# Performance work log

Measured on AMD Instinct MI355X. Metric: run time of the kernel, lower is better.

## Reference

```python
import jax, jax.numpy as jnp
import numpy as np

H = 16          # num_heads
BASE = 10000.0  # lrpe base
EPS = 1e-6      # rmsnorm eps


def setup_inputs() -> dict:
    key = jax.random.key(0)
    ks = jax.random.split(key, 8)
    b, n, d = 2, 2048, 1024
    hd = d // H
    s = 1.0 / np.sqrt(d)
    x = jax.random.normal(ks[0], (b, n, d), jnp.float32)
    wq = jax.random.normal(ks[1], (d, d), jnp.float32) * s
    wk = jax.random.normal(ks[2], (d, d), jnp.float32) * s
    wv = jax.random.normal(ks[3], (d, d), jnp.float32) * s
    wo = jax.random.normal(ks[4], (d, d), jnp.float32) * s
    wg1 = jax.random.normal(ks[5], (d, hd), jnp.float32) * s
    wg2 = jax.random.normal(ks[6], (hd, d), jnp.float32) * (1.0 / np.sqrt(hd))
    norm_w = jnp.ones((d,), jnp.float32)
    return {"x": x, "wq": wq, "wk": wk, "wv": wv, "wo": wo,
            "wg1": wg1, "wg2": wg2, "norm_w": norm_w}


def reference(x, wq, wk, wv, wo, wg1, wg2, norm_w):
    b, n, d = x.shape
    hd = d // H
    # projections + activations
    q = jax.nn.silu(x @ wq).reshape(b, n, H, hd)
    k = (x @ wk).reshape(b, n, H, hd)
    v = (x @ wv).reshape(b, n, H, hd)
    # vector decay via logcumsumexp over time (lse_state starts at 0 -> z[:,0]=0)
    f = jnp.concatenate([jnp.zeros((b, 1, H, hd), x.dtype), k], axis=1)  # (b,n+1,h,d)
    z = jax.lax.cumlogsumexp(f, axis=1)
    log_f = z[:, :-1] - z[:, 1:]          # (b,n,h,d), <= 0
    k = jnp.exp(k - z[:, 1:])             # normalized exp kernel keys
    # LRPE type 1 (cosine): d -> 2d, per-head theta slice
    theta = BASE ** (-2.0 / (H * hd) * jnp.arange(H * hd, dtype=x.dtype))
    theta = theta.reshape(H, hd)
    ang = jnp.arange(n, dtype=x.dtype)[:, None, None] * theta[None]  # (n,h,d)
    c, s_ = jnp.cos(ang), jnp.sin(ang)
    q = jnp.concatenate([q * c, q * s_], axis=-1)   # (b,n,h,2d)
    k = jnp.concatenate([k * c, k * s_], axis=-1)
    ld = jnp.concatenate([log_f, log_f], axis=-1)   # repeat '... d -> ... (g d)', g=2
    # lightning linear attention with vector decay: S_t = diag(exp(ld_t)) S_{t-1} + k_t v_t^T
    def step(S, inp):
        qt, kt, vt, lt = inp
        S = jnp.exp(lt)[..., None] * S + kt[..., None] * vt[..., None, :]
        o = jnp.einsum('bhe,bhev->bhv', qt, S)
        return S, o
    S0 = jnp.zeros((b, H, 2 * hd, hd), x.dtype)
    seq = (jnp.moveaxis(q, 1, 0), jnp.moveaxis(k, 1, 0),
           jnp.moveaxis(v, 1, 0), jnp.moveaxis(ld, 1, 0))
    _, o = jax.lax.scan(step, S0, seq)
    o = jnp.moveaxis(o, 0, 1).reshape(b, n, d)
    # fused gated group-RMSNorm (gate_pos='pre', sigmoid gate, num_groups=H)
    gate = (x @ wg1) @ wg2
    g = o * jax.nn.sigmoid(gate)
    gg = g.reshape(b, n, H, hd)
    rms = jnp.sqrt(jnp.mean(gg * gg, axis=-1, keepdims=True) + EPS)
    normed = (gg / rms).reshape(b, n, d) * norm_w
    return normed @ wo
```

## Files before the change

kernel.cpp:

```cpp
#include <hip/hip_runtime.h>
#include <math.h>

#define NH 16
#define HD 64
#define DMODEL 1024
#define NSEQ 2048
#define BATCH 2
#define CHUNK 32
#define NCH (NSEQ / CHUNK)
#define LN_BASE 9.210340371976184f

typedef __attribute__((ext_vector_type(8))) short bf16x8;
typedef __attribute__((ext_vector_type(8))) unsigned short u16x8;
typedef __attribute__((ext_vector_type(4))) float f32x4;

__device__ __forceinline__ unsigned short f2bf(float f) {
  union { float f; unsigned int u; } v; v.f = f;
  unsigned int u = v.u;
  unsigned int r = u + 0x7FFFu + ((u >> 16) & 1u);
  return (unsigned short)(r >> 16);
}
__device__ __forceinline__ float bf2f(unsigned short u) {
  union { unsigned int u; float f; } v; v.u = ((unsigned int)u) << 16;
  return v.f;
}

__device__ __forceinline__ void fast_sincos(float ang, float* s, float* c) {
  const float INV2PI = 0.15915494309189535f;
  const float TWOPI  = 6.283185307179586f;
  float rev = ang * INV2PI;
  rev = rev - floorf(rev);
  float ar = rev * TWOPI;
  *s = __sinf(ar);
  *c = __cosf(ar);
}

__device__ __forceinline__ void gload_lds16(const unsigned short* g,
                                            unsigned short* l) {
  __builtin_amdgcn_global_load_lds(
      (const __attribute__((address_space(1))) void*)g,
      (__attribute__((address_space(3))) void*)l, 16, 0, 0);
}

__global__ __launch_bounds__(256) void transpose_cvt6(
    const float* __restrict__ s0, const float* __restrict__ s1,
    const float* __restrict__ s2, const float* __restrict__ s3,
    const float* __restrict__ s4, const float* __restrict__ xs,
    unsigned short* __restrict__ d0, unsigned short* __restrict__ d1,
    unsigned short* __restrict__ d2, unsigned short* __restrict__ d3,
    unsigned short* __restrict__ d4, unsigned short* __restrict__ xd) {
  const int z = blockIdx.z;
  if (z == 5) {
    const int lin = blockIdx.y * 32 + blockIdx.x;
    const size_t base = (size_t)lin * 4096 + threadIdx.x * 4;
#pragma unroll
    for (int r = 0; r < 4; ++r) {
      float4 v = *(const float4*)(xs + base + r * 1024);
      unsigned short* o = xd + base + r * 1024;
      o[0] = f2bf(v.x); o[1] = f2bf(v.y); o[2] = f2bf(v.z); o[3] = f2bf(v.w);
    }
    return;
  }
  const float* in = (z == 0) ? s0 : (z == 1) ? s1 : (z == 2) ? s2
                    : (z == 3) ? s3 : s4;
  unsigned short* out = (z == 0) ? d0 : (z == 1) ? d1 : (z == 2) ? d2
                        : (z == 3) ? d3 : d4;
  __shared__ float tl[32][33];
  const int t = threadIdx.x;
  const int ci = t & 31, ri = t >> 5;
  const int br = blockIdx.y * 32, bc = blockIdx.x * 32;
#pragma unroll
  for (int rr = 0; rr < 4; ++rr)
    tl[ri + rr * 8][ci] = in[(size_t)(br + ri + rr * 8) * DMODEL + bc + ci];
  __syncthreads();
#pragma unroll
  for (int rr = 0; rr < 4; ++rr) {
    const int orow = bc + ri + rr * 8;
    const int ocol = br + ci;
    out[(size_t)orow * DMODEL + ocol] = f2bf(tl[ci][ri + rr * 8]);
  }
}

__global__ __launch_bounds__(256) void wg_gemm(const float* __restrict__ A,
                                               const float* __restrict__ B,
                                               float* __restrict__ C) {
  __shared__ float As[64][65];
  __shared__ float Bs[64][64];
  const int tid = threadIdx.x;
  const int tx = tid & 15, ty = tid >> 4;
  const int bm = (blockIdx.x >> 4) * 64;
  const int bn = (blockIdx.x & 15) * 64;

  {
    const int row = tid >> 2;
    const int ko = (tid & 3) * 16;
    const float* src = A + (size_t)(bm + row) * 64 + ko;
#pragma unroll
    for (int q = 0; q < 4; ++q) {
      float4 v = *(const float4*)(src + q * 4);
      As[row][ko + q * 4 + 0] = v.x; As[row][ko + q * 4 + 1] = v.y;
      As[row][ko + q * 4 + 2] = v.z; As[row][ko + q * 4 + 3] = v.w;
    }
  }
  {
    const int k = tid >> 2;
    const int co = (tid & 3) * 16;
    const float* src = B + (size_t)k * DMODEL + bn + co;
#pragma unroll
    for (int q = 0; q < 4; ++q)
      *(float4*)&Bs[k][co + q * 4] = *(const float4*)(src + q * 4);
  }
  __syncthreads();

  float acc[4][4];
#pragma unroll
  for (int i = 0; i < 4; ++i)
#pragma unroll
    for (int j = 0; j < 4; ++j) acc[i][j] = 0.f;
#pragma unroll 8
  for (int kk = 0; kk < 64; ++kk) {
    float a[4], b[4];
#pragma unroll
    for (int i = 0; i < 4; ++i) a[i] = As[ty * 4 + i][kk];
#pragma unroll
    for (int j = 0; j < 4; ++j) b[j] = Bs[kk][tx * 4 + j];
#pragma unroll
    for (int i = 0; i < 4; ++i)
#pragma unroll
      for (int j = 0; j < 4; ++j) acc[i][j] = fmaf(a[i], b[j], acc[i][j]);
  }
#pragma unroll
  for (int i = 0; i < 4; ++i) {
    float4 r = make_float4(acc[i][0], acc[i][1], acc[i][2], acc[i][3]);
    *(float4*)&C[(size_t)(bm + ty * 4 + i) * DMODEL + bn + tx * 4] = r;
  }
}

__global__ __launch_bounds__(256, 6) void gemm_bf16_fused(
    const unsigned short* __restrict__ A, const unsigned short* __restrict__ Bt,
    unsigned short* __restrict__ B0, unsigned short* __restrict__ B1,
    unsigned short* __restrict__ B2, unsigned short* __restrict__ B3,
    int M, int Ntot, int K) {
  __shared__ unsigned short As[64][64];
  __shared__ unsigned short Bs[128][64];
  const int tid = threadIdx.x;
  const int l = tid & 63;
  const int w = tid >> 6;
  const int wr = (w >> 1) * 32;
  const int wc = (w & 1) * 64;

  const int orig = blockIdx.x;
  const int xcd = orig & 7;
  const int idx = orig >> 3;
  const int bm = ((xcd >> 1) * 16 + (idx & 15)) * 64;
  const int bn = ((xcd & 1) * 16 + (idx >> 4)) * 128;

  const int lrow = l >> 3;
  const int cd = l & 7;
  const int cl = cd ^ lrow;

  f32x4 acc[2][4];
#pragma unroll
  for (int m = 0; m < 2; ++m)
#pragma unroll
    for (int n = 0; n < 4; ++n) acc[m][n] = (f32x4){0.f, 0.f, 0.f, 0.f};

  for (int k0 = 0; k0 < K; k0 += 64) {
    __syncthreads();
#pragma unroll
    for (int c = 0; c < 2; ++c) {
      const int row = w * 16 + c * 8 + lrow;
      unsigned short* la = (unsigned short*)As + (w * 16 + c * 8) * 64 + l * 8;
      gload_lds16(A + (size_t)(bm + row) * K + k0 + cl * 8, la);
    }
#pragma unroll
    for (int c = 0; c < 4; ++c) {
      const int row = w * 32 + c * 8 + lrow;
      unsigned short* lb = (unsigned short*)Bs + (w * 32 + c * 8) * 64 + l * 8;
      gload_lds16(Bt + (size_t)(bn + row) * K + k0 + cl * 8, lb);
    }
    __syncthreads();

#pragma unroll
    for (int ks = 0; ks < 2; ++ks) {
      bf16x8 af[2], bfr[4];
#pragma unroll
      for (int m = 0; m < 2; ++m) {
        const int r = wr + m * 16 + (l & 15);
        const int phys = (ks * 4 + (l >> 4)) ^ (r & 7);
        af[m] = *(const bf16x8*)&As[r][phys * 8];
      }
#pragma unroll
      for (int n = 0; n < 4; ++n) {
        const int r = wc + n * 16 + (l & 15);
        const int phys = (ks * 4 + (l >> 4)) ^ (r & 7);
        bfr[n] = *(const bf16x8*)&Bs[r][phys * 8];
      }
#pragma unroll
      for (int m = 0; m < 2; ++m)
#pragma unroll
        for (int n = 0; n < 4; ++n)
          acc[m][n] = __builtin_amdgcn_mfma_f32_16x16x32_bf16(af[m], bfr[n], acc[m][n], 0, 0, 0);
    }
  }

#pragma unroll
  for (int m = 0; m < 2; ++m) {
    const int row0 = bm + wr + m * 16 + (l >> 4) * 4;
#pragma unroll
    for (int n = 0; n < 4; ++n) {
      const int colw = wc + n * 16 + (l & 15);
#pragma unroll
      for (int r = 0; r < 4; ++r) {
        float x = acc[m][n][r];
        const int nb = bn >> 10;
        unsigned short* Bb = (nb == 0) ? B0 : (nb == 1) ? B1 : (nb == 2) ? B2 : B3;
        const int col = (bn & 1023) + colw;
        if (nb == 0) x = x / (1.f + expf(-x));
        Bb[(size_t)(row0 + r) * DMODEL + col] = f2bf(x);
      }
    }
  }
}

__global__ __launch_bounds__(256, 6) void gemm_bf16_wo(
    const unsigned short* __restrict__ A, const unsigned short* __restrict__ Bt,
    float* __restrict__ C, int M, int N, int K) {
  __shared__ unsigned short As[32][64];
  __shared__ unsigned short Bs[128][64];
  const int tid = threadIdx.x;
  const int l = tid & 63;
  const int w = tid >> 6;
  const int wr = (w >> 1) * 16;
  const int wc = (w & 1) * 64;

  const int nwg = gridDim.x;
  const int orig = blockIdx.x;
  const int swz = (orig & 7) * (nwg >> 3) + (orig >> 3);
  const int ntn = N >> 7;
  const int bm = (swz / ntn) * 32;
  const int bn = (swz % ntn) * 128;

  const int lrow = l >> 3;
  const int cd = l & 7;
  const int cl = cd ^ lrow;

  f32x4 acc[4];
#pragma unroll
  for (int n = 0; n < 4; ++n) acc[n] = (f32x4){0.f, 0.f, 0.f, 0.f};

  for (int k0 = 0; k0 < K; k0 += 64) {
    __syncthreads();
    {
      const int row = w * 8 + lrow;
      unsigned short* la = (unsigned short*)As + (w * 8) * 64 + l * 8;
      gload_lds16(A + (size_t)(bm + row) * K + k0 + cl * 8, la);
    }
#pragma unroll
    for (int c = 0; c < 4; ++c) {
      const int row = w * 32 + c * 8 + lrow;
      unsigned short* lb = (unsigned short*)Bs + (w * 32 + c * 8) * 64 + l * 8;
      gload_lds16(Bt + (size_t)(bn + row) * K + k0 + cl * 8, lb);
    }
    __syncthreads();

#pragma unroll
    for (int ks = 0; ks < 2; ++ks) {
      bf16x8 af, bfr[4];
      {
        const int r = wr + (l & 15);
        const int phys = (ks * 4 + (l >> 4)) ^ (r & 7);
        af = *(const bf16x8*)&As[r][phys * 8];
      }
#pragma unroll
      for (int n = 0; n < 4; ++n) {
        const int r = wc + n * 16 + (l & 15);
        const int phys = (ks * 4 + (l >> 4)) ^ (r & 7);
        bfr[n] = *(const bf16x8*)&Bs[r][phys * 8];
      }
#pragma unroll
      for (int n = 0; n < 4; ++n)
        acc[n] = __builtin_amdgcn_mfma_f32_16x16x32_bf16(af, bfr[n], acc[n], 0, 0, 0);
    }
  }

  {
    const int row0 = bm + wr + (l >> 4) * 4;
#pragma unroll
    for (int n = 0; n < 4; ++n) {
      const int col = bn + wc + n * 16 + (l & 15);
#pragma unroll
      for (int r = 0; r < 4; ++r)
        C[(size_t)(row0 + r) * N + col] = acc[n][r];
    }
  }
}

template <int ACT>
__global__ __launch_bounds__(256) void gemm_f32(const float* __restrict__ A,
                                                const float* __restrict__ B,
                                                float* __restrict__ C,
                                                int M, int N, int K) {
  __shared__ __align__(16) float As[16][128];
  __shared__ __align__(16) float Bs[16][128];
  const int tid = threadIdx.x;
  const int tx = tid & 15;
  const int ty = tid >> 4;
  const int bm = blockIdx.y * 128;
  const int bn = blockIdx.x * 128;

  float acc[8][8];
#pragma unroll
  for (int i = 0; i < 8; ++i)
#pragma unroll
    for (int j = 0; j < 8; ++j) acc[i][j] = 0.f;

  for (int k0 = 0; k0 < K; k0 += 16) {
    {
      const int row = tid >> 1;
      const int ko = (tid & 1) * 8;
      const float* src = A + (size_t)(bm + row) * K + k0 + ko;
      float4 a0 = *(const float4*)src;
      float4 a1 = *(const float4*)(src + 4);
      As[ko + 0][row] = a0.x; As[ko + 1][row] = a0.y;
      As[ko + 2][row] = a0.z; As[ko + 3][row] = a0.w;
      As[ko + 4][row] = a1.x; As[ko + 5][row] = a1.y;
      As[ko + 6][row] = a1.z; As[ko + 7][row] = a1.w;
    }
    {
      const int kr = tid >> 4;
      const int no = (tid & 15) * 8;
      float4 b0 = make_float4(0.f, 0.f, 0.f, 0.f);
      float4 b1 = b0;
      if (no < N) {
        const float* src = B + (size_t)(k0 + kr) * N + bn + no;
        b0 = *(const float4*)src;
        b1 = *(const float4*)(src + 4);
      }
      *(float4*)&Bs[kr][no] = b0;
      *(float4*)&Bs[kr][no + 4] = b1;
    }
    __syncthreads();
#pragma unroll
    for (int kk = 0; kk < 16; ++kk) {
      float a[8], b[8];
      *(float4*)&a[0] = *(const float4*)&As[kk][ty * 8];
      *(float4*)&a[4] = *(const float4*)&As[kk][ty * 8 + 4];
      *(float4*)&b[0] = *(const float4*)&Bs[kk][tx * 8];
      *(float4*)&b[4] = *(const float4*)&Bs[kk][tx * 8 + 4];
#pragma unroll
      for (int i = 0; i < 8; ++i)
#pragma unroll
        for (int j = 0; j < 8; ++j) acc[i][j] = fmaf(a[i], b[j], acc[i][j]);
    }
    __syncthreads();
  }

#pragma unroll
  for (int i = 0; i < 8; ++i) {
    const int row = bm + ty * 8 + i;
#pragma unroll
    for (int j = 0; j < 8; j += 4) {
      const int col = bn + tx * 8 + j;
      if (col < N) {
        float4 r;
        float* rv = (float*)&r;
#pragma unroll
        for (int q = 0; q < 4; ++q) {
          float x = acc[i][j + q];
          if (ACT == 1) x = x / (1.f + expf(-x));
          rv[q] = x;
        }
        *(float4*)&C[(size_t)row * N + col] = r;
      }
    }
  }
}

__global__ __launch_bounds__(256) void chunk_partial(
    const unsigned short* __restrict__ kb, float* __restrict__ partial) {
  const int blk = blockIdx.x;
  const int b = blk >> 8;
  const int rem = blk & 255;
  const int c = rem >> 2;
  const int seg = rem & 3;
  const int ch = seg * 256 + threadIdx.x;
  const unsigned short* base = kb + ((size_t)(b * NSEQ + c * CHUNK)) * DMODEL + ch;
  float acc = 0.f;
  for (int s = 0; s < CHUNK; ++s)
    acc += expf(bf2f(base[(size_t)s * DMODEL]));
  partial[((size_t)(b * NCH + c)) * DMODEL + ch] = acc;
}

__global__ __launch_bounds__(256) void chunk_zoff(const float* __restrict__ partial,
                                                  float* __restrict__ zoff) {
  const int g = blockIdx.x * 256 + threadIdx.x;
  const int b = g >> 10, dd = g & 1023;
  const size_t base = (size_t)b * NCH * DMODEL + dd;
  float vals[NCH];
#pragma unroll
  for (int c = 0; c < NCH; ++c)
    vals[c] = partial[base + (size_t)c * DMODEL];
  float run = 1.0f;
#pragma unroll
  for (int c = 0; c < NCH; ++c) {
    zoff[base + (size_t)c * DMODEL] = run;
    run += vals[c];
  }
}

__global__ __launch_bounds__(256) void chunk_attn(
    const unsigned short* __restrict__ qb, const unsigned short* __restrict__ kb,
    const unsigned short* __restrict__ vb, const float* __restrict__ zoff,
    unsigned short* __restrict__ qp, unsigned short* __restrict__ G,
    unsigned short* __restrict__ ob) {
  const int bidx = blockIdx.x;
  const int bh = bidx / NCH, c = bidx % NCH;
  const int b = bh >> 4, h = bh & 15;
  const int c0 = h * HD;

  __shared__ float sk[CHUNK][64];
  __shared__ float ps[4][64];
  __shared__ __align__(16) unsigned short qplds[CHUNK][136];
  __shared__ __align__(16) unsigned short khlds[CHUNK][136];
  __shared__ __align__(16) unsigned short kht[128][40];
  __shared__ __align__(16) unsigned short vt[64][40];
  __shared__ __align__(16) unsigned short slds[CHUNK][40];

  const int tid = threadIdx.x;
  const int l = tid & 63;
  const int w = tid >> 6;

  for (int idx = tid; idx < CHUNK * 64; idx += 256) {
    const int s = idx >> 6, dd2 = idx & 63;
    const size_t g = ((size_t)(b * NSEQ + c * CHUNK + s)) * DMODEL + c0 + dd2;
    sk[s][dd2] = bf2f(kb[g]);
    vt[dd2][s] = vb[g];
  }
  __syncthreads();

  const int dd = l;
  const int wq_ = w;
  {
    float a = 0.f;
#pragma unroll
    for (int i = 0; i < CHUNK / 4; ++i) a += expf(sk[wq_ * (CHUNK / 4) + i][dd]);
    ps[wq_][dd] = a;
  }
  __syncthreads();
  {
    float z = zoff[((size_t)(b * NCH + c)) * DMODEL + c0 + dd];
    for (int q2 = 0; q2 < wq_; ++q2) z += ps[q2][dd];
    const float theta = expf(-2.0f * (float)(c0 + dd) * (1.0f / 1024.0f) * LN_BASE);
#pragma unroll 2
    for (int i = 0; i < CHUNK / 4; ++i) {
      const int s = wq_ * (CHUNK / 4) + i;
      const int t = c * CHUNK + s;
      const float ek = expf(sk[s][dd]);
      z += ek;
      float sn, cs_;
      fast_sincos((float)t * theta, &sn, &cs_);
      const float qv = bf2f(qb[((size_t)(b * NSEQ + t)) * DMODEL + c0 + dd]);
      const float inv = 1.0f / z;
      const unsigned short kcb = f2bf(ek * cs_);
      const unsigned short ksb = f2bf(ek * sn);
      const unsigned short qcb = f2bf(qv * cs_ * inv);
      const unsigned short qsb = f2bf(qv * sn * inv);
      khlds[s][dd] = kcb;
      khlds[s][64 + dd] = ksb;
      kht[dd][s] = kcb;
      kht[64 + dd][s] = ksb;
      qplds[s][dd] = qcb;
      qplds[s][64 + dd] = qsb;
      unsigned short* qpo = qp + ((size_t)bidx * CHUNK + s) * 128;
      qpo[dd] = qcb;
      qpo[64 + dd] = qsb;
    }
  }
  __syncthreads();

  {
    const int mw = w >> 1, nw = w & 1;
    f32x4 sd = (f32x4){0.f, 0.f, 0.f, 0.f};
#pragma unroll
    for (int ks = 0; ks < 4; ++ks) {
      bf16x8 aq = *(const bf16x8*)&qplds[mw * 16 + (l & 15)][(l >> 4) * 8 + ks * 32];
      bf16x8 bk = *(const bf16x8*)&khlds[nw * 16 + (l & 15)][(l >> 4) * 8 + ks * 32];
      sd = __builtin_amdgcn_mfma_f32_16x16x32_bf16(aq, bk, sd, 0, 0, 0);
    }
    const int trow = mw * 16 + (l >> 4) * 4;
    const int scol = nw * 16 + (l & 15);
#pragma unroll
    for (int r = 0; r < 4; ++r) {
      const float v = (scol <= trow + r) ? sd[r] : 0.f;
      slds[trow + r][scol] = f2bf(v);
    }
  }

  {
    unsigned short* go = G + (size_t)bidx * 8192;
    const bf16x8 bv = *(const bf16x8*)&vt[w * 16 + (l & 15)][(l >> 4) * 8];
    const int jc = w * 16 + (l & 15);
#pragma unroll
    for (int et = 0; et < 8; ++et) {
      bf16x8 ak = *(const bf16x8*)&kht[et * 16 + (l & 15)][(l >> 4) * 8];
      f32x4 gd = (f32x4){0.f, 0.f, 0.f, 0.f};
      gd = __builtin_amdgcn_mfma_f32_16x16x32_bf16(ak, bv, gd, 0, 0, 0);
      const int e0r = et * 16 + (l >> 4) * 4;
#pragma unroll
      for (int r = 0; r < 4; ++r) go[(e0r + r) * 64 + jc] = f2bf(gd[r]);
    }
  }
  __syncthreads();

  {
    const bf16x8 bv = *(const bf16x8*)&vt[w * 16 + (l & 15)][(l >> 4) * 8];
    const int jc = w * 16 + (l & 15);
#pragma unroll
    for (int tt = 0; tt < 2; ++tt) {
      bf16x8 as = *(const bf16x8*)&slds[tt * 16 + (l & 15)][(l >> 4) * 8];
      f32x4 od = (f32x4){0.f, 0.f, 0.f, 0.f};
      od = __builtin_amdgcn_mfma_f32_16x16x32_bf16(as, bv, od, 0, 0, 0);
      const int trow = tt * 16 + (l >> 4) * 4;
#pragma unroll
      for (int r = 0; r < 4; ++r)
        ob[((size_t)(b * NSEQ + c * CHUNK + trow + r)) * DMODEL + c0 + jc] = f2bf(od[r]);
    }
  }
}

__global__ __launch_bounds__(256) void chunk_prefix(unsigned short* __restrict__ G) {
  const int g = blockIdx.x * 256 + threadIdx.x;
  const int bh = g >> 12;
  const int e2 = (g & 4095) * 2;
  unsigned int* base = (unsigned int*)(G + (size_t)bh * NCH * 8192 + e2);
  unsigned int vals[NCH];
#pragma unroll
  for (int c = 0; c < NCH; ++c)
    vals[c] = base[(size_t)c * 4096];
  float run0 = 0.f, run1 = 0.f;
#pragma unroll
  for (int c = 0; c < NCH; ++c) {
    base[(size_t)c * 4096] =
        (unsigned int)f2bf(run0) | ((unsigned int)f2bf(run1) << 16);
    run0 += bf2f((unsigned short)(vals[c] & 0xFFFFu));
    run1 += bf2f((unsigned short)(vals[c] >> 16));
  }
}

__global__ __launch_bounds__(256) void chunk_inter_norm(
    const unsigned short* __restrict__ qp, const unsigned short* __restrict__ S0,
    const unsigned short* __restrict__ ob, const unsigned short* __restrict__ gate,
    const float* __restrict__ norm_w, unsigned short* __restrict__ outb) {
  const int bidx = blockIdx.x;
  const int bh = bidx / NCH, c = bidx % NCH;
  const int b = bh >> 4, h = bh & 15;
  const int c0 = h * HD;

  __shared__ float s0l[128][68];
  __shared__ float qpl[CHUNK][132];

  const int tid = threadIdx.x;
  {
    const unsigned short* src = S0 + (size_t)bidx * 8192;
    for (int idx = tid * 8; idx < 8192; idx += 2048) {
      const int e = idx >> 6, j = idx & 63;
      u16x8 v8 = *(const u16x8*)(src + idx);
#pragma unroll
      for (int q = 0; q < 8; ++q) s0l[e][j + q] = bf2f(v8[q]);
    }
    const unsigned short* qsrc = qp + (size_t)bidx * CHUNK * 128;
    for (int idx = tid * 8; idx < CHUNK * 128; idx += 2048) {
      const int t = idx >> 7, e = idx & 127;
      u16x8 v8 = *(const u16x8*)(qsrc + idx);
#pragma unroll
      for (int q = 0; q < 8; ++q) qpl[t][e + q] = bf2f(v8[q]);
    }
  }
  __syncthreads();

  const int t = tid >> 3;
  const int j0 = (tid & 7) * 8;
  float acc[8] = {0, 0, 0, 0, 0, 0, 0, 0};
#pragma unroll 4
  for (int e = 0; e < 128; ++e) {
    const float a = qpl[t][e];
#pragma unroll
    for (int j = 0; j < 8; ++j) acc[j] = fmaf(a, s0l[e][j0 + j], acc[j]);
  }

  const size_t rowoff = ((size_t)(b * NSEQ + c * CHUNK + t)) * DMODEL + c0 + j0;
  u16x8 oi = *(const u16x8*)(ob + rowoff);
  u16x8 gt = *(const u16x8*)(gate + rowoff);
  float g[8];
  float ss = 0.f;
#pragma unroll
  for (int q = 0; q < 8; ++q) {
    const float o = acc[q] + bf2f(oi[q]);
    const float gv = bf2f(gt[q]);
    g[q] = o / (1.f + expf(-gv));
    ss = fmaf(g[q], g[q], ss);
  }
  ss += __shfl_xor(ss, 1);
  ss += __shfl_xor(ss, 2);
  ss += __shfl_xor(ss, 4);
  const float rms = sqrtf(ss * (1.0f / 64.0f) + 1e-6f);
  const float inv = 1.0f / rms;
  u16x8 outv;
#pragma unroll
  for (int q = 0; q < 8; ++q)
    outv[q] = f2bf(g[q] * inv * norm_w[c0 + j0 + q]);
  *(u16x8*)(outb + rowoff) = outv;
}

__global__ __launch_bounds__(256) void scan_kernel(const float* __restrict__ qb,
                                                   const float* __restrict__ kb,
                                                   const float* __restrict__ vb,
                                                   float* __restrict__ ob) {
  const int bh = blockIdx.x;
  const int b = bh >> 4;
  const int h = bh & 15;
  const int c0 = h * HD;

  __shared__ float sk[64][64];
  __shared__ float sq[64][64];
  __shared__ float sv[64][64];
  __shared__ float kh[128];
  __shared__ float qph[128];
  __shared__ float vsh[64];
  __shared__ float opart[4][64];

  const int tid = threadIdx.x;
  const int lane = tid & 63;
  const int w = tid >> 6;
  const int e0 = w * 32;

  float T[32];
#pragma unroll
  for (int i = 0; i < 32; ++i) T[i] = 0.f;

  float zrun = 1.0f;
  float theta_v = 0.f;
  if (tid < 64) theta_v = expf(-2.0f * (float)(c0 + tid) * (1.0f / 1024.0f) * LN_BASE);

  for (int t0 = 0; t0 < NSEQ; t0 += 64) {
    __syncthreads();
    for (int idx = tid; idx < 64 * 64; idx += 256) {
      const int tl = idx >> 6;
      const int dd = idx & 63;
      const size_t g = ((size_t)(b * NSEQ + t0 + tl)) * DMODEL + c0 + dd;
      sk[tl][dd] = kb[g];
      sq[tl][dd] = qb[g];
      sv[tl][dd] = vb[g];
    }
    __syncthreads();

    for (int tl = 0; tl < 64; ++tl) {
      const int t = t0 + tl;
      if (tid < 64) {
        const int dd = tid;
        const float kr = sk[tl][dd];
        const float ek = expf(kr);
        zrun += ek;
        const float inv = 1.0f / zrun;
        float cs_, sn;
        fast_sincos((float)t * theta_v, &sn, &cs_);
        const float qv = sq[tl][dd];
        kh[dd] = ek * cs_;
        kh[64 + dd] = ek * sn;
        qph[dd] = qv * cs_ * inv;
        qph[64 + dd] = qv * sn * inv;
        vsh[dd] = sv[tl][dd];
      }
      __syncthreads();

      const float vj = vsh[lane];
      float accj = 0.f;
#pragma unroll
      for (int i = 0; i < 32; ++i) {
        T[i] = fmaf(kh[e0 + i], vj, T[i]);
        accj = fmaf(qph[e0 + i], T[i], accj);
      }
      opart[w][lane] = accj;
      __syncthreads();

      if (tid < 64) {
        const float o = opart[0][tid] + opart[1][tid] + opart[2][tid] + opart[3][tid];
        ob[((size_t)(b * NSEQ + t)) * DMODEL + c0 + tid] = o;
      }
    }
  }
}

__global__ __launch_bounds__(256) void gated_rmsnorm_f32(
    const float* __restrict__ o, const float* __restrict__ gate,
    const float* __restrict__ norm_w, float* __restrict__ outf) {
  const int gidx = blockIdx.x * 4 + (threadIdx.x >> 6);
  const int lane = threadIdx.x & 63;
  const size_t base = (size_t)gidx * 64 + lane;
  const float ov = o[base];
  const float gv = gate[base];
  const float g = ov / (1.f + expf(-gv));
  float ss = g * g;
#pragma unroll
  for (int off = 32; off; off >>= 1) ss += __shfl_xor(ss, off);
  const float rms = sqrtf(ss * (1.0f / 64.0f) + 1e-6f);
  const int cch = (gidx & 15) * 64 + lane;
  outf[base] = g / rms * norm_w[cch];
}

extern "C" void kernel_launch(void* const* d_in, const int* in_sizes, int n_in,
                              void* d_out, int out_size, void* d_ws, size_t ws_size,
                              hipStream_t stream) {
  const float* x      = (const float*)d_in[0];
  const float* wq     = (const float*)d_in[1];
  const float* wk     = (const float*)d_in[2];
  const float* wv     = (const float*)d_in[3];
  const float* wo     = (const float*)d_in[4];
  const float* wg1    = (const float*)d_in[5];
  const float* wg2    = (const float*)d_in[6];
  const float* norm_w = (const float*)d_in[7];
  float* out = (float*)d_out;

  const int M = BATCH * NSEQ;
  const size_t SZ = (size_t)M * DMODEL;
  const size_t WSZ = (size_t)DMODEL * DMODEL;

  float* qbuf = (float*)d_ws;
  float* kbuf = qbuf + SZ;
  float* vbuf = kbuf + SZ;
  float* obuf = vbuf + SZ;
  float* gbuf = obuf + SZ;
  float* g1   = gbuf + SZ;
  float* part = g1 + (size_t)M * HD;
  float* zoff = part + (size_t)BATCH * NCH * DMODEL;
  float* qpb  = zoff + (size_t)BATCH * NCH * DMODEL;
  float* Gb   = qpb + (size_t)BATCH * NH * NCH * CHUNK * 128;
  float* f32_end = Gb + (size_t)BATCH * NH * NCH * 8192;

  unsigned short* xbf   = (unsigned short*)f32_end;
  unsigned short* wAll  = xbf + SZ;
  unsigned short* wqT   = wAll;
  unsigned short* wkT   = wAll + WSZ;
  unsigned short* wvT   = wAll + 2 * WSZ;
  unsigned short* WgT   = wAll + 3 * WSZ;
  unsigned short* woT   = wAll + 4 * WSZ;
  unsigned short* nrmbf = woT + WSZ;
  unsigned short* u16_end = nrmbf + SZ;

  const size_t need_full = (size_t)((char*)u16_end - (char*)d_ws);

  unsigned short* qbuf16 = (unsigned short*)qbuf;
  unsigned short* kbuf16 = (unsigned short*)kbuf;
  unsigned short* vbuf16 = (unsigned short*)vbuf;
  unsigned short* obuf16 = (unsigned short*)obuf;
  unsigned short* gbuf16 = (unsigned short*)gbuf;
  unsigned short* qpb16  = (unsigned short*)qpb;
  unsigned short* Gb16   = (unsigned short*)Gb;

  float* Wg = Gb;

  dim3 blk(256);
  dim3 grid_d((DMODEL + 127) / 128, (M + 127) / 128);
  dim3 grid_g1(1, (M + 127) / 128);

  const bool full_ok = ws_size >= need_full;

  if (full_ok) {
    wg_gemm<<<dim3(256), blk, 0, stream>>>(wg1, wg2, Wg);
    transpose_cvt6<<<dim3(DMODEL / 32, DMODEL / 32, 6), blk, 0, stream>>>(
        wq, wk, wv, wo, Wg, x, wqT, wkT, wvT, woT, WgT, xbf);
    gemm_bf16_fused<<<dim3((M / 64) * (4 * DMODEL / 128)), blk, 0, stream>>>(
        xbf, wAll, qbuf16, kbuf16, vbuf16, gbuf16, M, 4 * DMODEL, DMODEL);

    chunk_partial<<<dim3(BATCH * NCH * 4), blk, 0, stream>>>(kbuf16, part);
    chunk_zoff<<<dim3(8), blk, 0, stream>>>(part, zoff);
    chunk_attn<<<dim3(BATCH * NH * NCH), blk, 0, stream>>>(qbuf16, kbuf16, vbuf16,
                                                           zoff, qpb16, Gb16, obuf16);
    chunk_prefix<<<dim3(BATCH * NH * 8192 / 512), blk, 0, stream>>>(Gb16);
    chunk_inter_norm<<<dim3(BATCH * NH * NCH), blk, 0, stream>>>(
        qpb16, Gb16, obuf16, gbuf16, norm_w, nrmbf);

    gemm_bf16_wo<<<dim3((M / 32) * (DMODEL / 128)), blk, 0, stream>>>(
        nrmbf, woT, out, M, DMODEL, DMODEL);
  } else {
    gemm_f32<1><<<grid_d, blk, 0, stream>>>(x, wq, qbuf, M, DMODEL, DMODEL);
    gemm_f32<0><<<grid_d, blk, 0, stream>>>(x, wk, kbuf, M, DMODEL, DMODEL);
    gemm_f32<0><<<grid_d, blk, 0, stream>>>(x, wv, vbuf, M, DMODEL, DMODEL);
    gemm_f32<0><<<grid_g1, blk, 0, stream>>>(x, wg1, g1, M, HD, DMODEL);
    gemm_f32<0><<<grid_d, blk, 0, stream>>>(g1, wg2, gbuf, M, DMODEL, HD);
    scan_kernel<<<dim3(BATCH * NH), blk, 0, stream>>>(qbuf, kbuf, vbuf, obuf);
    float* nrm = kbuf;
    gated_rmsnorm_f32<<<dim3(M * NH / 4), blk, 0, stream>>>(obuf, gbuf, norm_w, nrm);
    gemm_f32<0><<<grid_d, blk, 0, stream>>>(nrm, wo, out, M, DMODEL, DMODEL);
  }
}
```

Before: 147.1 us.

## Use MFMA for inter-chunk state product and store chunk states transposed

The intra-chunk kernel now writes each per-chunk K^T V state transposed (j-major, e contiguous) as packed 64-bit bf16 stores. The inter-chunk/norm kernel then reads Q' and the transposed state straight from global memory into bf16 MFMA operands, replacing the LDS-staged scalar FMA loop over 128 features. The RMS reduction is reworked to match the MFMA output layout, using lane shuffles plus a small shared array to combine the two wave halves. This is meant to cut the ALU and LDS cost of the Q·S0 product. In exchange, the final outputs are written as scattered 2-byte stores instead of 16-byte vectors.

```diff
diff --git a/kernel.cpp b/kernel.cpp
--- a/kernel.cpp
+++ b/kernel.cpp
@@ -507,8 +507,12 @@
       f32x4 gd = (f32x4){0.f, 0.f, 0.f, 0.f};
       gd = __builtin_amdgcn_mfma_f32_16x16x32_bf16(ak, bv, gd, 0, 0, 0);
       const int e0r = et * 16 + (l >> 4) * 4;
-#pragma unroll
-      for (int r = 0; r < 4; ++r) go[(e0r + r) * 64 + jc] = f2bf(gd[r]);
+      unsigned long long pk =
+          (unsigned long long)f2bf(gd[0])
+        | ((unsigned long long)f2bf(gd[1]) << 16)
+        | ((unsigned long long)f2bf(gd[2]) << 32)
+        | ((unsigned long long)f2bf(gd[3]) << 48);
+      *(unsigned long long*)(go + (size_t)jc * 128 + e0r) = pk;
     }
   }
   __syncthreads();
@@ -549,7 +553,7 @@
 }
 
 __global__ __launch_bounds__(256) void chunk_inter_norm(
-    const unsigned short* __restrict__ qp, const unsigned short* __restrict__ S0,
+    const unsigned short* __restrict__ qp, const unsigned short* __restrict__ S0t,
     const unsigned short* __restrict__ ob, const unsigned short* __restrict__ gate,
     const float* __restrict__ norm_w, unsigned short* __restrict__ outb) {
   const int bidx = blockIdx.x;
@@ -557,60 +561,73 @@
   const int b = bh >> 4, h = bh & 15;
   const int c0 = h * HD;
 
-  __shared__ float s0l[128][68];
-  __shared__ float qpl[CHUNK][132];
-
   const int tid = threadIdx.x;
-  {
-    const unsigned short* src = S0 + (size_t)bidx * 8192;
-    for (int idx = tid * 8; idx < 8192; idx += 2048) {
-      const int e = idx >> 6, j = idx & 63;
-      u16x8 v8 = *(const u16x8*)(src + idx);
-#pragma unroll
-      for (int q = 0; q < 8; ++q) s0l[e][j + q] = bf2f(v8[q]);
-    }
-    const unsigned short* qsrc = qp + (size_t)bidx * CHUNK * 128;
-    for (int idx = tid * 8; idx < CHUNK * 128; idx += 2048) {
-      const int t = idx >> 7, e = idx & 127;
-      u16x8 v8 = *(const u16x8*)(qsrc + idx);
-#pragma unroll
-      for (int q = 0; q < 8; ++q) qpl[t][e + q] = bf2f(v8[q]);
-    }
+  const int l = tid & 63;
+  const int w = tid >> 6;
+  const int mw = w >> 1;
+  const int nw = w & 1;
+
+  const unsigned short* qpb = qp + (size_t)bidx * CHUNK * 128;
+  const unsigned short* s0b = S0t + (size_t)bidx * 8192;
+
+  f32x4 acc[2];
+  acc[0] = (f32x4){0.f, 0.f, 0.f, 0.f};
+  acc[1] = (f32x4){0.f, 0.f, 0.f, 0.f};
+#pragma unroll
+  for (int ks = 0; ks < 4; ++ks) {
+    const int ko = ks * 32 + (l >> 4) * 8;
+    bf16x8 xa = *(const bf16x8*)(qpb + (size_t)(mw * 16 + (l & 15)) * 128 + ko);
+#pragma unroll
+    for (int n = 0; n < 2; ++n) {
+      const int j = (nw * 2 + n) * 16 + (l & 15);
+      bf16x8 yb = *(const bf16x8*)(s0b + (size_t)j * 128 + ko);
+      acc[n] = __builtin_amdgcn_mfma_f32_16x16x32_bf16(xa, yb, acc[n], 0, 0, 0);
+    }
+  }
+
+  __shared__ float ssh[2][32];
+  float gval[2][4];
+  float ssr[4];
+#pragma unroll
+  for (int r = 0; r < 4; ++r) {
+    ssr[r] = 0.f;
+    const int row = mw * 16 + (l >> 4) * 4 + r;
+    const size_t rowg = ((size_t)(b * NSEQ + c * CHUNK + row)) * DMODEL + c0;
+#pragma unroll
+    for (int n = 0; n < 2; ++n) {
+      const int col = (nw * 2 + n) * 16 + (l & 15);
+      const float o = acc[n][r] + bf2f(ob[rowg + col]);
+      const float gv = bf2f(gate[rowg + col]);
+      const float g = o / (1.f + expf(-gv));
+      gval[n][r] = g;
+      ssr[r] = fmaf(g, g, ssr[r]);
+    }
+  }
+#pragma unroll
+  for (int r = 0; r < 4; ++r) {
+    ssr[r] += __shfl_xor(ssr[r], 1);
+    ssr[r] += __shfl_xor(ssr[r], 2);
+    ssr[r] += __shfl_xor(ssr[r], 4);
+    ssr[r] += __shfl_xor(ssr[r], 8);
+  }
+  if ((l & 15) == 0) {
+#pragma unroll
+    for (int r = 0; r < 4; ++r)
+      ssh[nw][mw * 16 + (l >> 4) * 4 + r] = ssr[r];
   }
   __syncthreads();
-
-  const int t = tid >> 3;
-  const int j0 = (tid & 7) * 8;
-  float acc[8] = {0, 0, 0, 0, 0, 0, 0, 0};
-#pragma unroll 4
-  for (int e = 0; e < 128; ++e) {
-    const float a = qpl[t][e];
-#pragma unroll
-    for (int j = 0; j < 8; ++j) acc[j] = fmaf(a, s0l[e][j0 + j], acc[j]);
-  }
-
-  const size_t rowoff = ((size_t)(b * NSEQ + c * CHUNK + t)) * DMODEL + c0 + j0;
-  u16x8 oi = *(const u16x8*)(ob + rowoff);
-  u16x8 gt = *(const u16x8*)(gate + rowoff);
-  float g[8];
-  float ss = 0.f;
-#pragma unroll
-  for (int q = 0; q < 8; ++q) {
-    const float o = acc[q] + bf2f(oi[q]);
-    const float gv = bf2f(gt[q]);
-    g[q] = o / (1.f + expf(-gv));
-    ss = fmaf(g[q], g[q], ss);
-  }
-  ss += __shfl_xor(ss, 1);
-  ss += __shfl_xor(ss, 2);
-  ss += __shfl_xor(ss, 4);
-  const float rms = sqrtf(ss * (1.0f / 64.0f) + 1e-6f);
-  const float inv = 1.0f / rms;
-  u16x8 outv;
-#pragma unroll
-  for (int q = 0; q < 8; ++q)
-    outv[q] = f2bf(g[q] * inv * norm_w[c0 + j0 + q]);
-  *(u16x8*)(outb + rowoff) = outv;
+#pragma unroll
+  for (int r = 0; r < 4; ++r) {
+    const int row = mw * 16 + (l >> 4) * 4 + r;
+    const float ss = ssr[r] + ssh[nw ^ 1][row];
+    const float inv = 1.0f / sqrtf(ss * (1.0f / 64.0f) + 1e-6f);
+    const size_t rowg = ((size_t)(b * NSEQ + c * CHUNK + row)) * DMODEL + c0;
+#pragma unroll
+    for (int n = 0; n < 2; ++n) {
+      const int col = (nw * 2 + n) * 16 + (l & 15);
+      outb[rowg + col] = f2bf(gval[n][r] * inv * norm_w[c0 + col]);
+    }
+  }
 }
 
 __global__ __launch_bounds__(256) void scan_kernel(const float* __restrict__ qb,
```

New measurement: 142.1 us. -3.4%, faster.
